# Kernel tuning notes

Hardware: AMD Instinct MI355X
Metric: run time of the kernel (lower is better)

## Reference

```python
import jax, jax.numpy as jnp
import numpy as np

B, L, D = 1, 2048, 1024
H, E = 16, 64        # n_heads, d_head
ROT = E // 2         # rotary half-dim
FF = 4 * D
EPS = 1e-6
NEG = -1e30


def setup_inputs() -> dict:
    key = jax.random.key(0)
    ks = jax.random.split(key, 6)
    x = jax.random.normal(ks[0], (B, L, D), jnp.float32)
    theta = jax.random.uniform(ks[1], (B, H, L, ROT), jnp.float32) * (2.0 * np.pi)
    scale = jax.random.normal(ks[2], (B, D), jnp.float32) * 0.1
    w_in = jax.random.normal(ks[3], (7 * D, D), jnp.float32) * (D ** -0.5)
    w_out = jax.random.normal(ks[4], (D, 5 * D), jnp.float32) * ((5 * D) ** -0.5)
    attn_scale = jnp.full((2, H), 10.0, jnp.float32)
    return {"x": x, "theta": theta, "scale": scale,
            "w_in": w_in, "w_out": w_out, "attn_scale": attn_scale}


def _rope(t, cos, sin):
    # t: [b,h,l,E]; rotary applied to first 2*ROT dims (== E here, so no passthrough)
    t1, t2 = t[..., :ROT], t[..., ROT:2 * ROT]
    return jnp.concatenate([t1 * cos - t2 * sin, t2 * cos + t1 * sin], axis=-1)


def _forward(x, theta, scale, w_in, w_out, attn_scale):
    b, l, d = x.shape
    skip = x
    # AdaRMSNorm (no learned weight): rms-normalize then modulate by (1 + scale)
    xn = x * jax.lax.rsqrt(jnp.mean(x ** 2, axis=-1, keepdims=True) + EPS)
    xn = xn * (1.0 + scale[:, None, :])
    # fused QKV + MLP-up projection (torch Linear: y = x @ W.T)
    proj = jnp.einsum('bld,fd->blf', xn, w_in)       # [b,l,7d]
    qkv, up = proj[..., :3 * d], proj[..., 3 * d:]
    up = jax.nn.gelu(up, approximate=True)           # GELU(tanh)
    # 'b l (t nh e) -> t b nh l e'
    qkv = qkv.reshape(b, l, 3, H, E).transpose(2, 0, 3, 1, 4)
    q, k, v = qkv[0], qkv[1], qkv[2]
    # cosine-sim rescaling: q_h * sqrt(s_h)/||q||, k_h * sqrt(s_h)/||k||
    s = jnp.sqrt(attn_scale[0])[None, :, None, None]
    q = q * (s * jax.lax.rsqrt(jnp.sum(q ** 2, axis=-1, keepdims=True) + EPS))
    k = k * (s * jax.lax.rsqrt(jnp.sum(k ** 2, axis=-1, keepdims=True) + EPS))
    # rotary embedding
    cos, sin = jnp.cos(theta), jnp.sin(theta)
    q, k = _rope(q, cos, sin), _rope(k, cos, sin)
    # causal attention with scale = 1.0 (cosine-sim path)
    scores = jnp.einsum('bhqe,bhke->bhqk', q, k)
    causal = jnp.tril(jnp.ones((l, l), bool))
    scores = jnp.where(causal[None, None], scores, NEG)
    probs = jax.nn.softmax(scores, axis=-1)
    attn = jnp.einsum('bhqk,bhke->bhqe', probs, v)
    attn_out = attn.transpose(0, 2, 1, 3).reshape(b, l, d)  # 'b nh l e -> b l (nh e)'
    h = jnp.concatenate([attn_out, up], axis=-1)            # [b,l,5d]
    return jnp.einsum('blf,df->bld', h, w_out) + skip


def reference(x, theta, scale, w_in, w_out, attn_scale):
    return _forward(x, theta, scale, w_in, w_out, attn_scale)
```

## Files before the change

### kernel.cpp

```cpp
#include <hip/hip_runtime.h>

typedef unsigned short u16;
typedef unsigned int u32;
typedef __attribute__((ext_vector_type(8))) short bf16x8;
typedef __attribute__((ext_vector_type(8))) unsigned short u16x8;
typedef __attribute__((ext_vector_type(4))) float f32x4;
typedef __attribute__((ext_vector_type(16))) float f32x16;

#define L_SEQ 2048
#define DMODEL 1024
#define NHEAD 16
#define EHEAD 64
#define FPROJ 7168
#define FCAT 5120
#define NEGINF -1e30f
#define LOG2E 1.44269504088896f
#define EXP2F(x) __builtin_amdgcn_exp2f(x)

__device__ __forceinline__ u16 f2bf(float f) {
  union { float f; u32 u; } v; v.f = f;
  u32 r = v.u + 0x7FFFu + ((v.u >> 16) & 1u);
  return (u16)(r >> 16);
}
__device__ __forceinline__ float bf2f(u16 h) {
  union { u32 u; float f; } v; v.u = ((u32)h) << 16;
  return v.f;
}
__device__ __forceinline__ float gelu_f(float x) {
  float y = 0.7978845608028654f * (x + 0.044715f * x * x * x);
  float t = __expf(-2.0f * fabsf(y));
  float th = (1.0f - t) / (1.0f + t);
  th = (y < 0.0f) ? -th : th;
  return 0.5f * x * (1.0f + th);
}
__device__ __forceinline__ void gld16(void* lds, const void* g) {
  __builtin_amdgcn_global_load_lds((const __attribute__((address_space(1))) u32*)g,
                                   (__attribute__((address_space(3))) u32*)lds, 16, 0, 0);
}

__global__ __launch_bounds__(256) void cvt2_kernel(const float* __restrict__ a,
                                                   u16* __restrict__ oa, int na4,
                                                   const float* __restrict__ b,
                                                   u16* __restrict__ ob, int nb4) {
  int i = blockIdx.x * 256 + threadIdx.x;
  const float* src;
  u16* dst;
  int j;
  if (i < na4) {
    src = a; dst = oa; j = i;
  } else {
    j = i - na4;
    if (j >= nb4) return;
    src = b; dst = ob;
  }
  float4 v = ((const float4*)src)[j];
  ((u32*)dst)[2 * j] = (u32)f2bf(v.x) | ((u32)f2bf(v.y) << 16);
  ((u32*)dst)[2 * j + 1] = (u32)f2bf(v.z) | ((u32)f2bf(v.w) << 16);
}

__global__ __launch_bounds__(256) void rmsnorm_kernel(const float* __restrict__ x,
                                                      const float* __restrict__ scale,
                                                      u16* __restrict__ xn) {
  int row = blockIdx.x;
  const float4 v = ((const float4*)(x + (size_t)row * DMODEL))[threadIdx.x];
  float ss = v.x * v.x + v.y * v.y + v.z * v.z + v.w * v.w;
#pragma unroll
  for (int m = 1; m < 64; m <<= 1) ss += __shfl_xor(ss, m);
  __shared__ float ws[4];
  if ((threadIdx.x & 63) == 0) ws[threadIdx.x >> 6] = ss;
  __syncthreads();
  float tot = ws[0] + ws[1] + ws[2] + ws[3];
  float r = rsqrtf(tot * (1.0f / DMODEL) + 1e-6f);
  float4 sc = ((const float4*)scale)[threadIdx.x];
  u32 w0 = (u32)f2bf(v.x * r * (1.0f + sc.x)) | ((u32)f2bf(v.y * r * (1.0f + sc.y)) << 16);
  u32 w1 = (u32)f2bf(v.z * r * (1.0f + sc.z)) | ((u32)f2bf(v.w * r * (1.0f + sc.w)) << 16);
  u32* dst = (u32*)(xn + (size_t)row * DMODEL);
  dst[2 * threadIdx.x] = w0;
  dst[2 * threadIdx.x + 1] = w1;
}

__device__ __forceinline__ void stage_half(u16* lds, const u16* g, int K, int tid) {
#pragma unroll
  for (int i = 0; i < 2; ++i) {
    int idx = tid + i * 512;
    int r = idx >> 3;
    int gcb = ((idx & 7) << 4) ^ ((r & 7) << 4);
    gld16((char*)lds + idx * 16, (const char*)g + (size_t)r * K * 2 + gcb);
  }
}

#define GFENCE asm volatile("" ::: "memory")
#define VMW1 asm volatile("s_waitcnt vmcnt(1)" ::: "memory")
#define VMW4 asm volatile("s_waitcnt vmcnt(4)" ::: "memory")
#define VMW6 asm volatile("s_waitcnt vmcnt(6)" ::: "memory")
#define ST_A(BUF, T, HALF) stage_half(sA + (BUF) * 16384 + (HALF) * 8192, \
    Ab + (size_t)((HALF) * 128) * K + (T) * 64, K, tid)
#define ST_B(BUF, T, HALF) stage_half(sB + (BUF) * 16384 + (HALF) * 8192, \
    Bb + (size_t)((HALF) * 128) * K + (T) * 64, K, tid)

#define PHASE(HM, KH, BUFB, WCODE, STCODE) do { \
    const char* ab_ = (const char*)sA + (BUFB) * 32768 + (HM) * 16384 + frow * 128 + ((KH) ? co1 : co0); \
    const char* bb_ = (const char*)sB + (BUFB) * 32768 + (wn * 32 + frow) * 128 + ((KH) ? co1 : co0); \
    bf16x8 af_[8], bv_[2]; \
    _Pragma("unroll") \
    for (int mr = 0; mr < 8; ++mr) af_[mr] = *(const bf16x8*)(ab_ + mr * 2048); \
    bv_[0] = *(const bf16x8*)(bb_); \
    bv_[1] = *(const bf16x8*)(bb_ + 2048); \
    GFENCE; \
    STCODE; \
    WCODE; \
    __builtin_amdgcn_s_barrier(); \
    __builtin_amdgcn_s_setprio(1); \
    _Pragma("unroll") \
    for (int mr = 0; mr < 8; ++mr) { \
      acc[(HM) * 8 + mr][0] = __builtin_amdgcn_mfma_f32_16x16x32_bf16(af_[mr], bv_[0], acc[(HM) * 8 + mr][0], 0, 0, 0); \
      acc[(HM) * 8 + mr][1] = __builtin_amdgcn_mfma_f32_16x16x32_bf16(af_[mr], bv_[1], acc[(HM) * 8 + mr][1], 0, 0, 0); \
    } \
    __builtin_amdgcn_s_setprio(0); \
    __builtin_amdgcn_s_barrier(); \
  } while (0)

template <int OUTMODE>
__global__ __launch_bounds__(512, 2) void gemm256(const u16* __restrict__ A,
                                                  const u16* __restrict__ B,
                                                  u16* __restrict__ C0,
                                                  u16* __restrict__ C1,
                                                  int M, int N, int K) {
  __shared__ __align__(16) u16 sA[2 * 16384];
  __shared__ __align__(16) u16 sB[2 * 16384];
  const int tid = threadIdx.x;
  const int lane = tid & 63;
  const int wn = tid >> 6;
  const int frow = lane & 15;
  const int kbyte = ((lane >> 4) & 3) << 4;
  const int sw = (frow & 7) << 4;
  const int co0 = kbyte ^ sw;
  const int co1 = (64 | kbyte) ^ sw;

  const int nbx = N >> 8;
  const int nbm = (int)gridDim.x / nbx;
  const int v = (blockIdx.x & 7) * ((int)gridDim.x >> 3) + ((int)blockIdx.x >> 3);
  const int bm = v % nbm, bn = v / nbm;
  const int kper = K / (int)gridDim.y;
  const int kbeg = blockIdx.y * kper;
  const u16* Ab = A + (size_t)(bm * 256) * K + kbeg;
  const u16* Bb = B + (size_t)(bn * 256) * K + kbeg;

  f32x4 acc[16][2] = {};

  const int NT = kper >> 6;
  ST_A(0, 0, 0); ST_B(0, 0, 0); ST_B(0, 0, 1); ST_A(0, 0, 1); ST_A(1, 1, 0);
  VMW1;
  __builtin_amdgcn_s_barrier();

  for (int kt = 0; kt < NT; kt += 2) {
    const int t1 = kt + 1;
    const int t2 = (kt + 2 >= NT) ? kt + 2 - NT : kt + 2;
    const int t3 = (kt + 3 >= NT) ? kt + 3 - NT : kt + 3;
    PHASE(0, 0, 0, , ST_B(1, t1, 0));
    PHASE(0, 1, 0, VMW6, ST_B(1, t1, 1));
    PHASE(1, 0, 0, , ST_A(1, t1, 1));
    PHASE(1, 1, 0, VMW4, ST_A(0, t2, 0));
    PHASE(0, 0, 1, , ST_B(0, t2, 0));
    PHASE(0, 1, 1, VMW6, ST_B(0, t2, 1));
    PHASE(1, 0, 1, , ST_A(0, t2, 1));
    PHASE(1, 1, 1, VMW4, ST_A(1, t3, 0));
  }

  if (OUTMODE == 1) {
    const bool up = (bn >= 12);
#pragma unroll
    for (int m16 = 0; m16 < 16; ++m16) {
#pragma unroll
      for (int nr = 0; nr < 2; ++nr) {
        int grow = bm * 256 + m16 * 16 + ((lane >> 4) * 4);
        int gcol = bn * 256 + wn * 32 + nr * 16 + frow;
        if (!up) {
          u16* cp = C0 + (size_t)grow * (3 * DMODEL) + gcol;
#pragma unroll
          for (int r = 0; r < 4; ++r) cp[(size_t)r * (3 * DMODEL)] = f2bf(acc[m16][nr][r]);
        } else {
          u16* cp = C1 + (size_t)grow * FCAT + (gcol - 2048);
#pragma unroll
          for (int r = 0; r < 4; ++r) cp[(size_t)r * FCAT] = f2bf(gelu_f(acc[m16][nr][r]));
        }
      }
    }
  } else {
    u16* Cp = C0 + (size_t)blockIdx.y * M * N;
#pragma unroll
    for (int m16 = 0; m16 < 16; ++m16) {
#pragma unroll
      for (int nr = 0; nr < 2; ++nr) {
        int grow = bm * 256 + m16 * 16 + ((lane >> 4) * 4);
        int gcol = bn * 256 + wn * 32 + nr * 16 + frow;
        u16* cp = Cp + (size_t)grow * N + gcol;
#pragma unroll
        for (int r = 0; r < 4; ++r) cp[(size_t)r * N] = f2bf(acc[m16][nr][r]);
      }
    }
  }
}

__global__ __launch_bounds__(256) void combine8(const u16* __restrict__ part,
                                                const float* __restrict__ x,
                                                float* __restrict__ out) {
  size_t i = (size_t)(blockIdx.x * 256 + threadIdx.x) * 8;
  float4 x0 = *(const float4*)(x + i);
  float4 x1 = *(const float4*)(x + i + 4);
  float s[8] = {x0.x, x0.y, x0.z, x0.w, x1.x, x1.y, x1.z, x1.w};
#pragma unroll
  for (int p = 0; p < 8; ++p) {
    u16x8 v = *(const u16x8*)(part + (size_t)p * (L_SEQ * DMODEL) + i);
#pragma unroll
    for (int j = 0; j < 8; ++j) s[j] += bf2f(v[j]);
  }
  float4 o0 = {s[0], s[1], s[2], s[3]};
  float4 o1 = {s[4], s[5], s[6], s[7]};
  *(float4*)(out + i) = o0;
  *(float4*)(out + i + 4) = o1;
}

__global__ __launch_bounds__(256) void qkv_prep(const u16* __restrict__ proj,
                                                const float* __restrict__ theta,
                                                const float* __restrict__ attn_scale,
                                                u16* __restrict__ qb, u16* __restrict__ kb,
                                                u16* __restrict__ vb) {
  const int l = blockIdx.x * 4 + (threadIdx.x >> 6);
  const int hd = blockIdx.y;
  const int e = threadIdx.x & 63;
  const u16* pr = proj + (size_t)l * (3 * DMODEL) + hd * EHEAD + e;
  float q = bf2f(pr[0]);
  float k = bf2f(pr[DMODEL]);
  float v = bf2f(pr[2 * DMODEL]);
  float sq = q * q, sk = k * k;
#pragma unroll
  for (int m = 1; m < 64; m <<= 1) {
    sq += __shfl_xor(sq, m);
    sk += __shfl_xor(sk, m);
  }
  float s = sqrtf(attn_scale[hd]);
  q *= LOG2E * s * rsqrtf(sq + 1e-6f);
  k *= s * rsqrtf(sk + 1e-6f);
  float ang = theta[((size_t)hd * L_SEQ + l) * 32 + (e & 31)];
  float cs = __cosf(ang), sn = __sinf(ang);
  float qp = __shfl_xor(q, 32), kp = __shfl_xor(k, 32);
  float qr = (e < 32) ? (q * cs - qp * sn) : (q * cs + qp * sn);
  float kr = (e < 32) ? (k * cs - kp * sn) : (k * cs + kp * sn);
  size_t o = ((size_t)hd * L_SEQ + l) * EHEAD + e;
  qb[o] = f2bf(qr);
  kb[o] = f2bf(kr);
  vb[o] = f2bf(v);
}

__global__ __launch_bounds__(128, 4) void attn_kernel(const u16* __restrict__ qb,
                                                      const u16* __restrict__ kb,
                                                      const u16* __restrict__ vb,
                                                      u16* __restrict__ po,
                                                      float* __restrict__ pm,
                                                      float* __restrict__ pl) {
  const int bid = blockIdx.x;
  const int s = 31 - (bid >> 6);
  const int hd = (bid >> 2) & 15;
  const int c = bid & 3;
  const int tid = threadIdx.x;
  const int lane = tid & 63;
  const int w = tid >> 6;
  const int h = lane >> 5;
  const int ql = lane & 31;
  const int qg = s * 64 + w * 32 + ql;
  const int nt = s + 1;
  const int t0 = (c * nt) >> 2;
  const int t1 = ((c + 1) * nt) >> 2;

  __shared__ u16 sK[64 * 64];
  __shared__ u16 sVT[64 * 64];

  const u16* Kh = kb + (size_t)hd * L_SEQ * EHEAD;
  const u16* Vh = vb + (size_t)hd * L_SEQ * EHEAD;
  const u16* Qh = qb + (size_t)hd * L_SEQ * EHEAD;

  bf16x8 qf[4];
#pragma unroll
  for (int es = 0; es < 4; ++es)
    qf[es] = *(const bf16x8*)(Qh + (size_t)qg * EHEAD + es * 16 + h * 8);

  f32x16 oa[2] = {};
  float m = NEGINF, lsum = 0.0f;

  const int vk = (tid & 15) * 4;
  const int ve = (tid >> 4) * 8;

  for (int kt = t0; kt < t1; ++kt) {
    const int k0 = kt * 64;
    __syncthreads();
#pragma unroll
    for (int i = 0; i < 4; ++i) {
      int r = w * 32 + i * 8 + (lane >> 3);
      const u16* src = Kh + (size_t)(k0 + r) * EHEAD + (((lane & 7) ^ (r & 7)) << 3);
      gld16(sK + (w * 32 + i * 8) * 64 + lane * 8, src);
    }
    u16x8 vr[4];
#pragma unroll
    for (int j = 0; j < 4; ++j)
      vr[j] = *(const u16x8*)(Vh + (size_t)(k0 + vk + j) * EHEAD + ve);
#pragma unroll
    for (int e = 0; e < 8; ++e) {
      int row = ve + e;
      int boff = row * 128 + ((((vk >> 3) ^ (row & 7)) << 4) | ((vk & 4) << 1));
      ushort4 pv;
      pv.x = vr[0][e]; pv.y = vr[1][e]; pv.z = vr[2][e]; pv.w = vr[3][e];
      *(ushort4*)((char*)sVT + boff) = pv;
    }
    __syncthreads();

    f32x16 st[2];
#pragma unroll
    for (int t = 0; t < 2; ++t) {
      f32x16 a = {};
      __builtin_amdgcn_s_setprio(1);
#pragma unroll
      for (int es = 0; es < 4; ++es) {
        int row = t * 32 + ql;
        int boff = row * 128 + (((es * 2 + h) ^ (row & 7)) << 4);
        bf16x8 kf = *(const bf16x8*)((const char*)sK + boff);
        a = __builtin_amdgcn_mfma_f32_32x32x16_bf16(kf, qf[es], a, 0, 0, 0);
      }
      __builtin_amdgcn_s_setprio(0);
      st[t] = a;
    }

    float p[2][16];
    float mx = NEGINF;
    const bool edge = (kt == s);
#pragma unroll
    for (int t = 0; t < 2; ++t)
#pragma unroll
      for (int r = 0; r < 16; ++r) {
        float v = st[t][r];
        if (edge) {
          int kg = k0 + t * 32 + (r & 3) + ((r >> 2) << 3) + h * 4;
          v = (kg > qg) ? NEGINF : v;
        }
        p[t][r] = v;
        mx = fmaxf(mx, v);
      }
    mx = fmaxf(mx, __shfl_xor(mx, 32));
    if (!__all(mx - m <= 8.0f)) {
      float mnew = fmaxf(m, mx);
      float alpha = EXP2F(m - mnew);
      lsum *= alpha;
#pragma unroll
      for (int et = 0; et < 2; ++et)
#pragma unroll
        for (int r = 0; r < 16; ++r) oa[et][r] *= alpha;
      m = mnew;
    }
    float ps = 0.0f;
#pragma unroll
    for (int t = 0; t < 2; ++t)
#pragma unroll
      for (int r = 0; r < 16; ++r) {
        float e_ = EXP2F(p[t][r] - m);
        p[t][r] = e_;
        ps += e_;
      }
    ps += __shfl_xor(ps, 32);
    lsum += ps;

    u32 pk_[2][8];
#pragma unroll
    for (int t = 0; t < 2; ++t)
#pragma unroll
      for (int i = 0; i < 8; ++i)
        asm("v_cvt_pk_bf16_f32 %0, %1, %2" : "=v"(pk_[t][i]) : "v"(p[t][2 * i]), "v"(p[t][2 * i + 1]));

#pragma unroll
    for (int ks = 0; ks < 4; ++ks) {
      const int tp = ks >> 1, base = (ks & 1) * 4;
      u32 s0 = h ? pk_[tp][base + 0] : pk_[tp][base + 2];
      u32 s1 = h ? pk_[tp][base + 1] : pk_[tp][base + 3];
      u32 r0 = (u32)__shfl_xor((int)s0, 32);
      u32 r1 = (u32)__shfl_xor((int)s1, 32);
      union { u32 u[4]; bf16x8 v; } pf;
      pf.u[0] = h ? r0 : pk_[tp][base + 0];
      pf.u[1] = h ? r1 : pk_[tp][base + 1];
      pf.u[2] = h ? pk_[tp][base + 2] : r0;
      pf.u[3] = h ? pk_[tp][base + 3] : r1;
      __builtin_amdgcn_s_setprio(1);
#pragma unroll
      for (int et = 0; et < 2; ++et) {
        int row = et * 32 + ql;
        int boff = row * 128 + (((ks * 2 + h) ^ (row & 7)) << 4);
        bf16x8 vf = *(const bf16x8*)((const char*)sVT + boff);
        oa[et] = __builtin_amdgcn_mfma_f32_32x32x16_bf16(vf, pf.v, oa[et], 0, 0, 0);
      }
      __builtin_amdgcn_s_setprio(0);
    }
  }

  const size_t pidx = (size_t)(s * 16 + hd) * 4 + c;
  u16* orow = po + pidx * 4096 + (size_t)(w * 32 + ql) * 64;
#pragma unroll
  for (int et = 0; et < 2; ++et)
#pragma unroll
    for (int g = 0; g < 4; ++g) {
      ushort4 ov;
      ov.x = f2bf(oa[et][4 * g + 0]);
      ov.y = f2bf(oa[et][4 * g + 1]);
      ov.z = f2bf(oa[et][4 * g + 2]);
      ov.w = f2bf(oa[et][4 * g + 3]);
      *(ushort4*)(orow + et * 32 + g * 8 + h * 4) = ov;
    }
  if (h == 0) {
    pm[pidx * 64 + w * 32 + ql] = m;
    pl[pidx * 64 + w * 32 + ql] = lsum;
  }
}

__global__ __launch_bounds__(256) void attn_merge(const u16* __restrict__ po,
                                                  const float* __restrict__ pm,
                                                  const float* __restrict__ pl,
                                                  u16* __restrict__ hb) {
  const int sh = blockIdx.x;
  const int s = sh >> 4, hd = sh & 15;
  const int r = threadIdx.x >> 2;
  const int ec = (threadIdx.x & 3) << 4;
  float mc[4], wgt[4];
  float M = NEGINF;
#pragma unroll
  for (int c = 0; c < 4; ++c) {
    mc[c] = pm[(size_t)(sh * 4 + c) * 64 + r];
    M = fmaxf(M, mc[c]);
  }
  float L = 0.0f;
#pragma unroll
  for (int c = 0; c < 4; ++c) {
    wgt[c] = EXP2F(mc[c] - M);
    L += pl[(size_t)(sh * 4 + c) * 64 + r] * wgt[c];
  }
  float inv = 1.0f / L;
  float o[16] = {};
#pragma unroll
  for (int c = 0; c < 4; ++c) {
    const u16* pp = po + (size_t)(sh * 4 + c) * 4096 + r * 64 + ec;
    u16x8 v0 = *(const u16x8*)pp;
    u16x8 v1 = *(const u16x8*)(pp + 8);
#pragma unroll
    for (int j = 0; j < 8; ++j) {
      o[j] += wgt[c] * bf2f(v0[j]);
      o[8 + j] += wgt[c] * bf2f(v1[j]);
    }
  }
  u16* dst = hb + (size_t)(s * 64 + r) * FCAT + hd * EHEAD + ec;
  u16x8 out0, out1;
#pragma unroll
  for (int j = 0; j < 8; ++j) {
    out0[j] = f2bf(o[j] * inv);
    out1[j] = f2bf(o[8 + j] * inv);
  }
  *(u16x8*)dst = out0;
  *(u16x8*)(dst + 8) = out1;
}

extern "C" void kernel_launch(void* const* d_in, const int* in_sizes, int n_in,
                              void* d_out, int out_size, void* d_ws, size_t ws_size,
                              hipStream_t stream) {
  const float* x = (const float*)d_in[0];
  const float* theta = (const float*)d_in[1];
  const float* scale = (const float*)d_in[2];
  const float* w_in = (const float*)d_in[3];
  const float* w_out = (const float*)d_in[4];
  const float* attn_scale = (const float*)d_in[5];
  float* out = (float*)d_out;

  char* ws = (char*)d_ws;
  u16* w_out_b = (u16*)ws;   ws += (size_t)DMODEL * FCAT * 2;
  u16* hb = (u16*)ws;        ws += (size_t)L_SEQ * FCAT * 2;
  u16* xn = (u16*)ws;        ws += (size_t)L_SEQ * DMODEL * 2;
  u16* w_in_b = (u16*)ws;    ws += (size_t)FPROJ * DMODEL * 2;
  u16* proj = (u16*)ws;      ws += (size_t)L_SEQ * 3 * DMODEL * 2;
  u16* qb = (u16*)ws;        ws += (size_t)NHEAD * L_SEQ * EHEAD * 2;
  u16* kb = (u16*)ws;        ws += (size_t)NHEAD * L_SEQ * EHEAD * 2;
  u16* vb = (u16*)ws;        ws += (size_t)NHEAD * L_SEQ * EHEAD * 2;
  u16* po = xn;
  float* pm = (float*)(po + (size_t)512 * 4 * 4096);
  float* pl = pm + 512 * 4 * 64;
  u16* part = xn;

  const int na4 = FPROJ * DMODEL / 4, nb4 = DMODEL * FCAT / 4;
  cvt2_kernel<<<(na4 + nb4 + 255) / 256, 256, 0, stream>>>(w_in, w_in_b, na4,
                                                           w_out, w_out_b, nb4);
  rmsnorm_kernel<<<L_SEQ, 256, 0, stream>>>(x, scale, xn);
  gemm256<1><<<(L_SEQ / 256) * (FPROJ / 256), 512, 0, stream>>>(xn, w_in_b, proj, hb,
                                                                L_SEQ, FPROJ, DMODEL);
  qkv_prep<<<dim3(L_SEQ / 4, NHEAD), 256, 0, stream>>>(proj, theta, attn_scale, qb, kb, vb);
  attn_kernel<<<2048, 128, 0, stream>>>(qb, kb, vb, po, pm, pl);
  attn_merge<<<512, 256, 0, stream>>>(po, pm, pl, hb);
  gemm256<2><<<dim3((L_SEQ / 256) * (DMODEL / 256), 8), 512, 0, stream>>>(hb, w_out_b, part,
                                                                          nullptr, L_SEQ, DMODEL, FCAT);
  combine8<<<L_SEQ * DMODEL / 8 / 256, 256, 0, stream>>>(part, x, out);
}
```

Before: 140.1 us.

## Use 2x4 wave tiling in GEMM with simplified double-buffered staging

Changes the 8-wave layout in the 256x256 GEMM from each wave owning a 256x32 strip to a 2x4 grid of 128x64 wave tiles. This cuts per-wave LDS fragment reads per MFMA: 8 A plus 4 B fragments feed 32 MFMAs, versus 8 A plus 2 B fragments feeding 16. The fine-grained 8-phase staging with partial vmcnt waits is replaced by a simple double buffer: each full next tile is issued in one phase, followed by a full vmcnt(0) wait. This reduces global-load and compute overlap and may expose memory latency.

Result: no change. 141.2 us (+0.8%).

```diff
diff --git a/kernel.cpp b/kernel.cpp
--- a/kernel.cpp
+++ b/kernel.cpp
@@ -90,32 +90,30 @@
 }
 
 #define GFENCE asm volatile("" ::: "memory")
-#define VMW1 asm volatile("s_waitcnt vmcnt(1)" ::: "memory")
-#define VMW4 asm volatile("s_waitcnt vmcnt(4)" ::: "memory")
-#define VMW6 asm volatile("s_waitcnt vmcnt(6)" ::: "memory")
+#define VMW0 asm volatile("s_waitcnt vmcnt(0)" ::: "memory")
 #define ST_A(BUF, T, HALF) stage_half(sA + (BUF) * 16384 + (HALF) * 8192, \
     Ab + (size_t)((HALF) * 128) * K + (T) * 64, K, tid)
 #define ST_B(BUF, T, HALF) stage_half(sB + (BUF) * 16384 + (HALF) * 8192, \
     Bb + (size_t)((HALF) * 128) * K + (T) * 64, K, tid)
 
-#define PHASE(HM, KH, BUFB, WCODE, STCODE) do { \
-    const char* ab_ = (const char*)sA + (BUFB) * 32768 + (HM) * 16384 + frow * 128 + ((KH) ? co1 : co0); \
-    const char* bb_ = (const char*)sB + (BUFB) * 32768 + (wn * 32 + frow) * 128 + ((KH) ? co1 : co0); \
-    bf16x8 af_[8], bv_[2]; \
+#define PHASE(KH, BUFB, WCODE, STCODE) do { \
+    const char* ab_ = (const char*)sA + (BUFB) * 32768 + wm * 16384 + frow * 128 + ((KH) ? co1 : co0); \
+    const char* bb_ = (const char*)sB + (BUFB) * 32768 + (wn2 >> 1) * 16384 + ((wn2 & 1) * 64 + frow) * 128 + ((KH) ? co1 : co0); \
+    bf16x8 af_[8], bv_[4]; \
     _Pragma("unroll") \
     for (int mr = 0; mr < 8; ++mr) af_[mr] = *(const bf16x8*)(ab_ + mr * 2048); \
-    bv_[0] = *(const bf16x8*)(bb_); \
-    bv_[1] = *(const bf16x8*)(bb_ + 2048); \
+    _Pragma("unroll") \
+    for (int nr = 0; nr < 4; ++nr) bv_[nr] = *(const bf16x8*)(bb_ + nr * 2048); \
     GFENCE; \
     STCODE; \
     WCODE; \
     __builtin_amdgcn_s_barrier(); \
     __builtin_amdgcn_s_setprio(1); \
     _Pragma("unroll") \
-    for (int mr = 0; mr < 8; ++mr) { \
-      acc[(HM) * 8 + mr][0] = __builtin_amdgcn_mfma_f32_16x16x32_bf16(af_[mr], bv_[0], acc[(HM) * 8 + mr][0], 0, 0, 0); \
-      acc[(HM) * 8 + mr][1] = __builtin_amdgcn_mfma_f32_16x16x32_bf16(af_[mr], bv_[1], acc[(HM) * 8 + mr][1], 0, 0, 0); \
-    } \
+    for (int mr = 0; mr < 8; ++mr) \
+      _Pragma("unroll") \
+      for (int nr = 0; nr < 4; ++nr) \
+        acc[mr][nr] = __builtin_amdgcn_mfma_f32_16x16x32_bf16(af_[mr], bv_[nr], acc[mr][nr], 0, 0, 0); \
     __builtin_amdgcn_s_setprio(0); \
     __builtin_amdgcn_s_barrier(); \
   } while (0)
@@ -130,7 +128,9 @@
   __shared__ __align__(16) u16 sB[2 * 16384];
   const int tid = threadIdx.x;
   const int lane = tid & 63;
-  const int wn = tid >> 6;
+  const int wv = tid >> 6;
+  const int wm = wv >> 2;
+  const int wn2 = wv & 3;
   const int frow = lane & 15;
   const int kbyte = ((lane >> 4) & 3) << 4;
   const int sw = (frow & 7) << 4;
@@ -146,57 +146,52 @@
   const u16* Ab = A + (size_t)(bm * 256) * K + kbeg;
   const u16* Bb = B + (size_t)(bn * 256) * K + kbeg;
 
-  f32x4 acc[16][2] = {};
+  f32x4 acc[8][4] = {};
 
   const int NT = kper >> 6;
-  ST_A(0, 0, 0); ST_B(0, 0, 0); ST_B(0, 0, 1); ST_A(0, 0, 1); ST_A(1, 1, 0);
-  VMW1;
+  ST_A(0, 0, 0); ST_A(0, 0, 1); ST_B(0, 0, 0); ST_B(0, 0, 1);
+  VMW0;
   __builtin_amdgcn_s_barrier();
 
   for (int kt = 0; kt < NT; kt += 2) {
     const int t1 = kt + 1;
-    const int t2 = (kt + 2 >= NT) ? kt + 2 - NT : kt + 2;
-    const int t3 = (kt + 3 >= NT) ? kt + 3 - NT : kt + 3;
-    PHASE(0, 0, 0, , ST_B(1, t1, 0));
-    PHASE(0, 1, 0, VMW6, ST_B(1, t1, 1));
-    PHASE(1, 0, 0, , ST_A(1, t1, 1));
-    PHASE(1, 1, 0, VMW4, ST_A(0, t2, 0));
-    PHASE(0, 0, 1, , ST_B(0, t2, 0));
-    PHASE(0, 1, 1, VMW6, ST_B(0, t2, 1));
-    PHASE(1, 0, 1, , ST_A(0, t2, 1));
-    PHASE(1, 1, 1, VMW4, ST_A(1, t3, 0));
+    const int t2 = (kt + 2 >= NT) ? 0 : kt + 2;
+    PHASE(0, 0, , ST_A(1, t1, 0); ST_A(1, t1, 1); ST_B(1, t1, 0); ST_B(1, t1, 1));
+    PHASE(1, 0, VMW0, );
+    PHASE(0, 1, , ST_A(0, t2, 0); ST_A(0, t2, 1); ST_B(0, t2, 0); ST_B(0, t2, 1));
+    PHASE(1, 1, VMW0, );
   }
 
   if (OUTMODE == 1) {
     const bool up = (bn >= 12);
 #pragma unroll
-    for (int m16 = 0; m16 < 16; ++m16) {
-#pragma unroll
-      for (int nr = 0; nr < 2; ++nr) {
-        int grow = bm * 256 + m16 * 16 + ((lane >> 4) * 4);
-        int gcol = bn * 256 + wn * 32 + nr * 16 + frow;
+    for (int mr = 0; mr < 8; ++mr) {
+#pragma unroll
+      for (int nr = 0; nr < 4; ++nr) {
+        int grow = bm * 256 + wm * 128 + mr * 16 + ((lane >> 4) * 4);
+        int gcol = bn * 256 + wn2 * 64 + nr * 16 + frow;
         if (!up) {
           u16* cp = C0 + (size_t)grow * (3 * DMODEL) + gcol;
 #pragma unroll
-          for (int r = 0; r < 4; ++r) cp[(size_t)r * (3 * DMODEL)] = f2bf(acc[m16][nr][r]);
+          for (int r = 0; r < 4; ++r) cp[(size_t)r * (3 * DMODEL)] = f2bf(acc[mr][nr][r]);
         } else {
           u16* cp = C1 + (size_t)grow * FCAT + (gcol - 2048);
 #pragma unroll
-          for (int r = 0; r < 4; ++r) cp[(size_t)r * FCAT] = f2bf(gelu_f(acc[m16][nr][r]));
+          for (int r = 0; r < 4; ++r) cp[(size_t)r * FCAT] = f2bf(gelu_f(acc[mr][nr][r]));
         }
       }
     }
   } else {
     u16* Cp = C0 + (size_t)blockIdx.y * M * N;
 #pragma unroll
-    for (int m16 = 0; m16 < 16; ++m16) {
-#pragma unroll
-      for (int nr = 0; nr < 2; ++nr) {
-        int grow = bm * 256 + m16 * 16 + ((lane >> 4) * 4);
-        int gcol = bn * 256 + wn * 32 + nr * 16 + frow;
+    for (int mr = 0; mr < 8; ++mr) {
+#pragma unroll
+      for (int nr = 0; nr < 4; ++nr) {
+        int grow = bm * 256 + wm * 128 + mr * 16 + ((lane >> 4) * 4);
+        int gcol = bn * 256 + wn2 * 64 + nr * 16 + frow;
         u16* cp = Cp + (size_t)grow * N + gcol;
 #pragma unroll
-        for (int r = 0; r < 4; ++r) cp[(size_t)r * N] = f2bf(acc[m16][nr][r]);
+        for (int r = 0; r < 4; ++r) cp[(size_t)r * N] = f2bf(acc[mr][nr][r]);
       }
     }
   }
```
